# Performance work log

Hardware: AMD Instinct MI355X
Metric: run time of the kernel (lower is better)

Reference implementation:

```python
import jax, jax.numpy as jnp
import numpy as np

N, E, B = 3000, 96000, 64
CIN, MID = 8, 16
G1, G2 = 32, 8
FC1, FC2, OUT = 512, 128, 10
EPS = 1e-5


def setup_inputs() -> dict:
    key = jax.random.key(0)
    ks = jax.random.split(key, 40)
    u = lambda k, shape, s: jax.random.uniform(k, shape, jnp.float32, -s, s)
    inp = {}
    inp['x'] = jax.random.normal(ks[0], (N, B, CIN), jnp.float32)
    inp['edge_index'] = jax.random.randint(ks[1], (2, E), 0, N, jnp.int64)
    # SAGEConv params (uniform(-1/sqrt(in_channels), ...))
    s = 1.0 / np.sqrt(CIN)
    inp['edge_w_raw'] = jnp.ones((E,), jnp.float32) * 0.01
    inp['sage_self_w'] = u(ks[2], (CIN, MID), s)
    inp['sage_w'] = u(ks[3], (CIN, MID), s)
    inp['sage_b'] = u(ks[4], (MID,), s)
    # LayerNorm over (num_nodes, mid_channel)
    inp['ln_g'] = jnp.ones((N, MID), jnp.float32)
    inp['ln_b'] = jnp.zeros((N, MID), jnp.float32)
    # 1x1 Conv2d stacks (stored as [out,in] matrices) + BatchNorm2d (eval stats)
    inp['conv1_w'] = jax.random.normal(ks[5], (G1, MID), jnp.float32) * np.sqrt(2.0 / G1)
    inp['conv1_b'] = u(ks[6], (G1,), 1.0 / np.sqrt(MID))
    inp['bn1_g'] = jax.random.uniform(ks[7], (G1,), jnp.float32, 0.5, 1.5)
    inp['bn1_b'] = jax.random.normal(ks[8], (G1,), jnp.float32) * 0.1
    inp['bn1_m'] = jax.random.normal(ks[9], (G1,), jnp.float32) * 0.1
    inp['bn1_v'] = jax.random.uniform(ks[10], (G1,), jnp.float32, 0.5, 1.5)
    inp['conv2_w'] = jax.random.normal(ks[11], (G2, G1), jnp.float32) * np.sqrt(2.0 / G2)
    inp['conv2_b'] = u(ks[12], (G2,), 1.0 / np.sqrt(G1))
    inp['bn2_g'] = jax.random.uniform(ks[13], (G2,), jnp.float32, 0.5, 1.5)
    inp['bn2_b'] = jax.random.normal(ks[14], (G2,), jnp.float32) * 0.1
    inp['bn2_m'] = jax.random.normal(ks[15], (G2,), jnp.float32) * 0.1
    inp['bn2_v'] = jax.random.uniform(ks[16], (G2,), jnp.float32, 0.5, 1.5)
    # FC stack: Linear(G2*N, FC1) + BN1d, Linear(FC1, FC2) + BN1d, fc1
    d0 = G2 * N
    inp['fc_w1'] = jax.random.normal(ks[17], (FC1, d0), jnp.float32) * np.sqrt(2.0 / (d0 + FC1))
    inp['fc_b1'] = jnp.full((FC1,), 0.01, jnp.float32)
    inp['bnf1_g'] = jax.random.uniform(ks[18], (FC1,), jnp.float32, 0.5, 1.5)
    inp['bnf1_b'] = jax.random.normal(ks[19], (FC1,), jnp.float32) * 0.1
    inp['bnf1_m'] = jax.random.normal(ks[20], (FC1,), jnp.float32) * 0.1
    inp['bnf1_v'] = jax.random.uniform(ks[21], (FC1,), jnp.float32, 0.5, 1.5)
    inp['fc_w2'] = jax.random.normal(ks[22], (FC2, FC1), jnp.float32) * np.sqrt(2.0 / (FC1 + FC2))
    inp['fc_b2'] = jnp.full((FC2,), 0.01, jnp.float32)
    inp['bnf2_g'] = jax.random.uniform(ks[23], (FC2,), jnp.float32, 0.5, 1.5)
    inp['bnf2_b'] = jax.random.normal(ks[24], (FC2,), jnp.float32) * 0.1
    inp['bnf2_m'] = jax.random.normal(ks[25], (FC2,), jnp.float32) * 0.1
    inp['bnf2_v'] = jax.random.uniform(ks[26], (FC2,), jnp.float32, 0.5, 1.5)
    inp['fc1_w'] = jax.random.normal(ks[27], (OUT, FC2), jnp.float32) * np.sqrt(2.0 / (FC2 + OUT))
    inp['fc1_b'] = jnp.full((OUT,), 0.01, jnp.float32)
    return inp


def _bn(y, g, b, m, v):
    # eval-mode BatchNorm; y is [B, C, N] or [B, C]
    if y.ndim == 3:
        return (y - m[:, None]) * (g[:, None] / jnp.sqrt(v[:, None] + EPS)) + b[:, None]
    return (y - m) * (g / jnp.sqrt(v + EPS)) + b


def reference(x, edge_index, edge_w_raw, sage_self_w, sage_w, sage_b, ln_g, ln_b,
              conv1_w, conv1_b, bn1_g, bn1_b, bn1_m, bn1_v,
              conv2_w, conv2_b, bn2_g, bn2_b, bn2_m, bn2_v,
              fc_w1, fc_b1, bnf1_g, bnf1_b, bnf1_m, bnf1_v,
              fc_w2, fc_b2, bnf2_g, bnf2_b, bnf2_m, bnf2_v,
              fc1_w, fc1_b):
    row, col = edge_index[0], edge_index[1]
    ew = jax.nn.sigmoid(edge_w_raw)
    # SAGEConv: gather -> weighted message -> scatter-mean by col -> matmul
    msg = x[row] * ew[:, None, None]                          # [E, B, CIN]
    summed = jax.ops.segment_sum(msg, col, num_segments=N)    # [N, B, CIN]
    cnt = jax.ops.segment_sum(jnp.ones((E,), x.dtype), col, num_segments=N)
    agg = summed / jnp.maximum(cnt, 1.0)[:, None, None]
    neigh = jnp.einsum('nbc,cm->nbm', agg, sage_w) + sage_b   # [N, B, MID]
    self_out = jnp.einsum('nbc,cm->nbm', x, sage_self_w)
    h = 0.0 * self_out + 1.0 * neigh                          # alphas = [0, 1]
    h = jax.nn.relu(h)
    # LayerNorm over (num_nodes, mid) per batch element
    hb = jnp.transpose(h, (1, 0, 2))                          # [B, N, MID]
    mu = hb.mean(axis=(1, 2), keepdims=True)
    var = hb.var(axis=(1, 2), keepdims=True)
    hb = (hb - mu) / jnp.sqrt(var + EPS) * ln_g + ln_b
    y = jnp.transpose(hb, (0, 2, 1))                          # [B, MID, N]
    # 1x1 conv stack (relu then BN, matching source order)
    y = jnp.einsum('om,bmn->bon', conv1_w, y) + conv1_b[:, None]
    y = _bn(jax.nn.relu(y), bn1_g, bn1_b, bn1_m, bn1_v)
    y = jnp.einsum('oc,bcn->bon', conv2_w, y) + conv2_b[:, None]
    y = _bn(jax.nn.relu(y), bn2_g, bn2_b, bn2_m, bn2_v)       # [B, G2, N]
    z = y.reshape(y.shape[0], -1)                             # [B, G2*N]
    z = jax.nn.relu(_bn(z @ fc_w1.T + fc_b1, bnf1_g, bnf1_b, bnf1_m, bnf1_v))
    z = jax.nn.relu(_bn(z @ fc_w2.T + fc_b2, bnf2_g, bnf2_b, bnf2_m, bnf2_v))
    logits = z @ fc1_w.T + fc1_b
    return jax.nn.softmax(logits, axis=-1), logits
```

## Files before the change

kernel.cpp:

```cpp
#include <hip/hip_runtime.h>
#include <hip/hip_bf16.h>
#include <math.h>

#define NN   3000
#define EE   96000
#define BB   64
#define CIN  8
#define MID  16
#define G1   32
#define G2   8
#define FC1N 512
#define FC2N 128
#define OUTN 10
#define EPSV 1e-5f

#define BC   (BB * CIN)
#define HROW (NN * MID)
#define D0   (G2 * NN)

#define P_EWRAW 0
#define P_SW    96000
#define P_SB    96128
#define P_LNG   96144
#define P_LNB   144144
#define P_C1W   192144
#define P_C1B   192656
#define P_BN1G  192688
#define P_BN1B  192720
#define P_BN1M  192752
#define P_BN1V  192784
#define P_C2W   192816
#define P_C2B   193072
#define P_BN2G  193080
#define P_BN2B  193088
#define P_BN2M  193096
#define P_BN2V  193104
#define P_FB1   193112
#define P_BF1G  193624
#define P_BF1B  194136
#define P_BF1M  194648
#define P_BF1V  195160
#define P_FW2   195672
#define P_FB2   261208
#define P_BF2G  261336
#define P_BF2B  261464
#define P_BF2M  261592
#define P_BF2V  261720
#define P_FOW   261848
#define P_FOB   263128
#define P_TOT   263138

#define KCH  320
#define NKC  75

__device__ __forceinline__ float b2f(unsigned short u) {
    union { unsigned int i; float f; } c;
    c.i = ((unsigned int)u) << 16;
    return c.f;
}
__device__ __forceinline__ unsigned short f2b_rne(float x) {
    union { float f; unsigned int u; } c; c.f = x;
    unsigned int r = c.u + 0x7FFFu + ((c.u >> 16) & 1u);
    return (unsigned short)(r >> 16);
}

typedef __attribute__((ext_vector_type(8))) short short8;
typedef __attribute__((ext_vector_type(4))) float f32x4;

struct PTab { const void* p[30]; };
__global__ __launch_bounds__(256)
void k_prep(const void* __restrict__ ei_raw, const unsigned int* __restrict__ ewr,
            PTab tab,
            int* __restrict__ ei32, int* __restrict__ cnt, int* __restrict__ flags,
            float* __restrict__ P) {
    __shared__ int sh_is64, sh_bf;
    if (threadIdx.x == 0) {
        const int* pw = (const int*)ei_raw;
        int any = 0;
        #pragma unroll
        for (int i = 1; i < 32; i += 2) any |= pw[i];
        sh_is64 = (any == 0) ? 1 : 0;
        unsigned int w = ewr[0];
        sh_bf = ((w >> 16) == (w & 0xFFFFu)) ? 1 : 0;
        if (blockIdx.x == 0) flags[0] = sh_bf;
    }
    __syncthreads();
    int bf = sh_bf;
    long long gi = (long long)blockIdx.x * blockDim.x + threadIdx.x;
    if (gi < 2 * EE) {
        int i = (int)gi;
        int v = sh_is64 ? (int)((const long long*)ei_raw)[i]
                        : ((const int*)ei_raw)[i];
        ei32[i] = v;
        if (i >= EE) atomicAdd(&cnt[v], 1);
        return;
    }
    gi -= 2 * EE;
    if (gi >= P_TOT) return;
    int i = (int)gi;
    const int off[31] = {
        P_EWRAW, P_SW, P_SB, P_LNG, P_LNB, P_C1W, P_C1B, P_BN1G, P_BN1B, P_BN1M,
        P_BN1V, P_C2W, P_C2B, P_BN2G, P_BN2B, P_BN2M, P_BN2V, P_FB1, P_BF1G,
        P_BF1B, P_BF1M, P_BF1V, P_FW2, P_FB2, P_BF2G, P_BF2B, P_BF2M, P_BF2V,
        P_FOW, P_FOB, P_TOT };
    int r = 0;
    #pragma unroll
    for (int j = 1; j < 31; ++j) r += (i >= off[j]) ? 1 : 0;
    int e = i - off[r];
    P[i] = bf ? b2f(((const unsigned short*)tab.p[r])[e])
              : ((const float*)tab.p[r])[e];
}

__global__ void k_scan(const int* __restrict__ cnt, int* __restrict__ off,
                       int* __restrict__ cursor) {
    __shared__ int part[1024];
    int t = threadIdx.x;
    int base = t * 3;
    int c0 = 0, c1 = 0, c2 = 0;
    if (base     < NN) c0 = cnt[base];
    if (base + 1 < NN) c1 = cnt[base + 1];
    if (base + 2 < NN) c2 = cnt[base + 2];
    int s = c0 + c1 + c2;
    part[t] = s;
    __syncthreads();
    for (int d = 1; d < 1024; d <<= 1) {
        int v = (t >= d) ? part[t - d] : 0;
        __syncthreads();
        part[t] += v;
        __syncthreads();
    }
    int excl = part[t] - s;
    if (base < NN)     { off[base]     = excl;           cursor[base]     = excl; }
    if (base + 1 < NN) { off[base + 1] = excl + c0;      cursor[base + 1] = excl + c0; }
    if (base + 2 < NN) { off[base + 2] = excl + c0 + c1; cursor[base + 2] = excl + c0 + c1; }
    if (t == 1023) off[NN] = part[1023];
}

__global__ void k_scatter(const int* __restrict__ ei, const float* __restrict__ ew,
                          int* __restrict__ cursor,
                          int* __restrict__ rcsr, float* __restrict__ wcsr) {
    int e = blockIdx.x * blockDim.x + threadIdx.x;
    if (e < EE) {
        int p = atomicAdd(&cursor[ei[EE + e]], 1);
        rcsr[p] = ei[e];
        wcsr[p] = 1.f / (1.f + expf(-ew[e]));
    }
}

__global__ __launch_bounds__(256)
void k_agg_sage(const void* __restrict__ xraw, const int* __restrict__ flags,
                const int* __restrict__ off,
                const int* __restrict__ rcsr, const float* __restrict__ wcsr,
                const float* __restrict__ sw, const float* __restrict__ sb,
                float* __restrict__ hb,
                float* __restrict__ statsS, float* __restrict__ statsQ) {
    __shared__ float aggL[BC];
    __shared__ float swL[CIN * MID];
    __shared__ float sbL[MID];
    __shared__ float lnS[BB], lnQ[BB];
    int t = threadIdx.x;
    if (t < CIN * MID) swL[t] = sw[t];
    if (t < MID)       sbL[t] = sb[t];
    if (t < BB) { lnS[t] = 0.f; lnQ[t] = 0.f; }
    int bf = flags[0];
    float accS[4] = {0.f, 0.f, 0.f, 0.f};
    float accQ[4] = {0.f, 0.f, 0.f, 0.f};
    __syncthreads();
    for (int j = 0; j < 4; ++j) {
        int n = blockIdx.x * 4 + j;
        int k0 = off[n], k1 = off[n + 1];
        float a0 = 0.f, a1 = 0.f, b0 = 0.f, b1 = 0.f;
        int k = k0;
        if (bf) {
            const unsigned int* xu = (const unsigned int*)xraw;
            for (; k + 3 < k1; k += 4) {
                int   r0 = rcsr[k],     r1 = rcsr[k + 1];
                int   r2 = rcsr[k + 2], r3 = rcsr[k + 3];
                float w0 = wcsr[k],     w1 = wcsr[k + 1];
                float w2 = wcsr[k + 2], w3 = wcsr[k + 3];
                unsigned int u0 = xu[(size_t)r0 * 256 + t];
                unsigned int u1 = xu[(size_t)r1 * 256 + t];
                unsigned int u2 = xu[(size_t)r2 * 256 + t];
                unsigned int u3 = xu[(size_t)r3 * 256 + t];
                a0 += b2f((unsigned short)(u0 & 0xFFFFu)) * w0;
                a1 += b2f((unsigned short)(u0 >> 16))     * w0;
                b0 += b2f((unsigned short)(u1 & 0xFFFFu)) * w1;
                b1 += b2f((unsigned short)(u1 >> 16))     * w1;
                a0 += b2f((unsigned short)(u2 & 0xFFFFu)) * w2;
                a1 += b2f((unsigned short)(u2 >> 16))     * w2;
                b0 += b2f((unsigned short)(u3 & 0xFFFFu)) * w3;
                b1 += b2f((unsigned short)(u3 >> 16))     * w3;
            }
            for (; k < k1; ++k) {
                int r0 = rcsr[k];
                float w0 = wcsr[k];
                unsigned int u0 = xu[(size_t)r0 * 256 + t];
                a0 += b2f((unsigned short)(u0 & 0xFFFFu)) * w0;
                a1 += b2f((unsigned short)(u0 >> 16))     * w0;
            }
        } else {
            const float* x = (const float*)xraw;
            for (; k + 3 < k1; k += 4) {
                int   r0 = rcsr[k],     r1 = rcsr[k + 1];
                int   r2 = rcsr[k + 2], r3 = rcsr[k + 3];
                float w0 = wcsr[k],     w1 = wcsr[k + 1];
                float w2 = wcsr[k + 2], w3 = wcsr[k + 3];
                const float* xp0 = x + (size_t)r0 * BC;
                const float* xp1 = x + (size_t)r1 * BC;
                const float* xp2 = x + (size_t)r2 * BC;
                const float* xp3 = x + (size_t)r3 * BC;
                a0 += xp0[t] * w0;  a1 += xp0[t + 256] * w0;
                b0 += xp1[t] * w1;  b1 += xp1[t + 256] * w1;
                a0 += xp2[t] * w2;  a1 += xp2[t + 256] * w2;
                b0 += xp3[t] * w3;  b1 += xp3[t + 256] * w3;
            }
            for (; k < k1; ++k) {
                int r0 = rcsr[k];
                float w0 = wcsr[k];
                const float* xp0 = x + (size_t)r0 * BC;
                a0 += xp0[t] * w0;
                a1 += xp0[t + 256] * w0;
            }
        }
        float inv = 1.f / fmaxf((float)(k1 - k0), 1.f);
        __syncthreads();
        if (bf) {
            aggL[2 * t]     = (a0 + b0) * inv;
            aggL[2 * t + 1] = (a1 + b1) * inv;
        } else {
            aggL[t]       = (a0 + b0) * inv;
            aggL[t + 256] = (a1 + b1) * inv;
        }
        __syncthreads();
        #pragma unroll
        for (int r4 = 0; r4 < 4; ++r4) {
            int q = t + r4 * 256;
            int b = q >> 4, m = q & 15;
            float v = sbL[m];
            const float* ag = &aggL[b * CIN];
            #pragma unroll
            for (int c = 0; c < CIN; ++c) v += ag[c] * swL[c * MID + m];
            v = fmaxf(v, 0.f);
            hb[(size_t)b * HROW + n * MID + m] = v;
            accS[r4] += v;
            accQ[r4] += v * v;
        }
    }
    __syncthreads();
    #pragma unroll
    for (int r4 = 0; r4 < 4; ++r4) {
        int b = (t + r4 * 256) >> 4;
        atomicAdd(&lnS[b], accS[r4]);
        atomicAdd(&lnQ[b], accQ[r4]);
    }
    __syncthreads();
    if (t < BB) {
        atomicAdd(&statsS[t], lnS[t]);
        atomicAdd(&statsQ[t], lnQ[t]);
    }
}

__global__ __launch_bounds__(256)
void k_conv_stack(const float* __restrict__ hb,
                  const float* __restrict__ statsS, const float* __restrict__ statsQ,
                  const float* __restrict__ P, unsigned short* __restrict__ zT) {
    __shared__ float hbt[64 * 65];
    __shared__ float w1s[G1 * MID], w2s[G2 * G1];
    __shared__ float c1s[G1], s1[G1], t1[G1];
    __shared__ float c2s[G2], s2[G2], t2[G2];
    int t = threadIdx.x;
    int n0 = blockIdx.x * 4;
    for (int j = t; j < G1 * MID; j += 256) w1s[j] = P[P_C1W + j];
    if (t < G2 * G1)  w2s[t] = P[P_C2W + t];
    if (t < G1) {
        float s = P[P_BN1G + t] / sqrtf(P[P_BN1V + t] + EPSV);
        c1s[t] = P[P_C1B + t]; s1[t] = s; t1[t] = P[P_BN1B + t] - P[P_BN1M + t] * s;
    }
    if (t < G2) {
        float s = P[P_BN2G + t] / sqrtf(P[P_BN2V + t] + EPSV);
        c2s[t] = P[P_C2B + t]; s2[t] = s; t2[t] = P[P_BN2B + t] - P[P_BN2M + t] * s;
    }
    #pragma unroll
    for (int r = 0; r < 4; ++r) {
        int i = r * 256 + t;
        int b = i >> 4, q = i & 15;
        float4 v = *(const float4*)(hb + (size_t)b * HROW + n0 * MID + q * 4);
        int ld = b * 65 + q * 4;
        hbt[ld] = v.x; hbt[ld + 1] = v.y; hbt[ld + 2] = v.z; hbt[ld + 3] = v.w;
    }
    __syncthreads();
    int nl = t >> 6, b = t & 63;
    int n = n0 + nl;
    float mu = statsS[b] / (float)HROW;
    float var = statsQ[b] / (float)HROW - mu * mu;
    float rs = 1.f / sqrtf(var + EPSV);
    float tv[MID];
    #pragma unroll
    for (int m = 0; m < MID; ++m) {
        float g = P[P_LNG + n * MID + m], lb = P[P_LNB + n * MID + m];
        tv[m] = (hbt[b * 65 + nl * MID + m] - mu) * rs * g + lb;
    }
    float v1[G1];
    #pragma unroll
    for (int o = 0; o < G1; ++o) {
        float d = c1s[o];
        #pragma unroll
        for (int m = 0; m < MID; ++m) d += w1s[o * MID + m] * tv[m];
        d = fmaxf(d, 0.f);
        v1[o] = d * s1[o] + t1[o];
    }
    #pragma unroll
    for (int o2 = 0; o2 < G2; ++o2) {
        float d = c2s[o2];
        #pragma unroll
        for (int c = 0; c < G1; ++c) d += w2s[o2 * G1 + c] * v1[c];
        d = fmaxf(d, 0.f);
        zT[((size_t)(o2 * NN + n)) * BB + b] = f2b_rne(d * s2[o2] + t2[o2]);
    }
}

__global__ __launch_bounds__(256)
void k_fc1(const unsigned short* __restrict__ zT, const void* __restrict__ w1raw,
           const int* __restrict__ flags, float* __restrict__ out1p) {
    __shared__ unsigned int zs[64 * 20];
    int kc = blockIdx.y;
    int t = threadIdx.x;
    int lane = t & 63;
    int wv = t >> 6;
    int n = lane & 15;
    int q = lane >> 4;
    int fbase = blockIdx.x * 64 + wv * 16;
    int bf = flags[0];
    const size_t kcb = (size_t)kc * KCH;
    const float*          w1f = (const float*)w1raw;
    const unsigned short* w1b = (const unsigned short*)w1raw;

    f32x4 acc0 = {0.f, 0.f, 0.f, 0.f};
    f32x4 acc1 = {0.f, 0.f, 0.f, 0.f};
    f32x4 acc2 = {0.f, 0.f, 0.f, 0.f};
    f32x4 acc3 = {0.f, 0.f, 0.f, 0.f};

    int zb = t & 63;
    int kg = t >> 6;

    for (int ks = 0; ks < KCH / 32; ++ks) {
        size_t k0 = kcb + (size_t)ks * 32;
        const unsigned short* zsrc = zT + (k0 + kg * 8) * BB + zb;
        unsigned short zv[8];
        #pragma unroll
        for (int j = 0; j < 8; ++j) zv[j] = zsrc[j * BB];
        unsigned int pk0 = (unsigned int)zv[0] | ((unsigned int)zv[1] << 16);
        unsigned int pk1 = (unsigned int)zv[2] | ((unsigned int)zv[3] << 16);
        unsigned int pk2 = (unsigned int)zv[4] | ((unsigned int)zv[5] << 16);
        unsigned int pk3 = (unsigned int)zv[6] | ((unsigned int)zv[7] << 16);
        __syncthreads();
        *(uint4*)&zs[zb * 20 + kg * 4] = make_uint4(pk0, pk1, pk2, pk3);
        short8 av;
        if (bf) {
            av = *(const short8*)(w1b + (size_t)(fbase + n) * D0 + k0 + q * 8);
        } else {
            const float* wr = w1f + (size_t)(fbase + n) * D0 + k0 + q * 8;
            float4 wa = *(const float4*)wr;
            float4 wb = *(const float4*)(wr + 4);
            av[0] = (short)f2b_rne(wa.x); av[1] = (short)f2b_rne(wa.y);
            av[2] = (short)f2b_rne(wa.z); av[3] = (short)f2b_rne(wa.w);
            av[4] = (short)f2b_rne(wb.x); av[5] = (short)f2b_rne(wb.y);
            av[6] = (short)f2b_rne(wb.z); av[7] = (short)f2b_rne(wb.w);
        }
        __syncthreads();
        const char* zbase = (const char*)zs + q * 16;
        short8 bv0 = *(const short8*)(zbase + (0  + n) * 80);
        short8 bv1 = *(const short8*)(zbase + (16 + n) * 80);
        short8 bv2 = *(const short8*)(zbase + (32 + n) * 80);
        short8 bv3 = *(const short8*)(zbase + (48 + n) * 80);
        acc0 = __builtin_amdgcn_mfma_f32_16x16x32_bf16(av, bv0, acc0, 0, 0, 0);
        acc1 = __builtin_amdgcn_mfma_f32_16x16x32_bf16(av, bv1, acc1, 0, 0, 0);
        acc2 = __builtin_amdgcn_mfma_f32_16x16x32_bf16(av, bv2, acc2, 0, 0, 0);
        acc3 = __builtin_amdgcn_mfma_f32_16x16x32_bf16(av, bv3, acc3, 0, 0, 0);
    }
    float* op = out1p + ((size_t)kc * FC1N + fbase + q * 4) * BB + n;
    #pragma unroll
    for (int r = 0; r < 4; ++r) {
        op[r * BB +  0] = acc0[r];
        op[r * BB + 16] = acc1[r];
        op[r * BB + 32] = acc2[r];
        op[r * BB + 48] = acc3[r];
    }
}

__global__ void k_fc1_fin(const float* __restrict__ out1p, const float* __restrict__ P,
                          float* __restrict__ z1) {
    int i = blockIdx.x * blockDim.x + threadIdx.x;
    if (i < BB * FC1N) {
        int f = i >> 6, b = i & 63;
        float acc = 0.f;
        for (int kc = 0; kc < NKC; ++kc)
            acc += out1p[((size_t)kc * FC1N + f) * BB + b];
        acc += P[P_FB1 + f];
        float s = P[P_BF1G + f] / sqrtf(P[P_BF1V + f] + EPSV);
        acc = (acc - P[P_BF1M + f]) * s + P[P_BF1B + f];
        z1[b * FC1N + f] = fmaxf(acc, 0.f);
    }
}

__global__ __launch_bounds__(128)
void k_fc2head(const float* __restrict__ z1, const float* __restrict__ P,
               const int* __restrict__ flags, void* __restrict__ outv) {
    __shared__ float zsrc[FC1N];
    __shared__ float z2s[FC2N];
    __shared__ float lg[OUTN];
    __shared__ float red[2];
    int b = blockIdx.x, t = threadIdx.x;
    #pragma unroll
    for (int r = 0; r < 4; ++r) zsrc[t + r * 128] = z1[b * FC1N + t + r * 128];
    __syncthreads();
    {
        int f = t;
        const float4* wr = (const float4*)(P + P_FW2 + (size_t)f * FC1N);
        const float4* zr = (const float4*)zsrc;
        float acc = P[P_FB2 + f];
        for (int k = 0; k < FC1N / 4; ++k) {
            float4 wv = wr[k];
            float4 zv = zr[k];
            acc += wv.x * zv.x + wv.y * zv.y + wv.z * zv.z + wv.w * zv.w;
        }
        float s = P[P_BF2G + f] / sqrtf(P[P_BF2V + f] + EPSV);
        acc = (acc - P[P_BF2M + f]) * s + P[P_BF2B + f];
        z2s[f] = fmaxf(acc, 0.f);
    }
    __syncthreads();
    if (t < OUTN) {
        float acc = P[P_FOB + t];
        const float* wr = P + P_FOW + t * FC2N;
        for (int k = 0; k < FC2N; ++k) acc += wr[k] * z2s[k];
        lg[t] = acc;
    }
    __syncthreads();
    if (t == 0) {
        float mx = lg[0];
        for (int o = 1; o < OUTN; ++o) mx = fmaxf(mx, lg[o]);
        float s = 0.f;
        for (int o = 0; o < OUTN; ++o) s += expf(lg[o] - mx);
        red[0] = mx; red[1] = s;
    }
    __syncthreads();
    if (t < OUTN) {
        float p = expf(lg[t] - red[0]) / red[1];
        if (flags[0]) {
            __hip_bfloat16* o = (__hip_bfloat16*)outv;
            o[b * OUTN + t] = __float2bfloat16(p);
            o[BB * OUTN + b * OUTN + t] = __float2bfloat16(lg[t]);
        } else {
            float* o = (float*)outv;
            o[b * OUTN + t] = p;
            o[BB * OUTN + b * OUTN + t] = lg[t];
        }
    }
}

extern "C" void kernel_launch(void* const* d_in, const int* in_sizes, int n_in,
                              void* d_out, int out_size, void* d_ws, size_t ws_size,
                              hipStream_t stream) {
    char* ws = (char*)d_ws;
    size_t o = 0;
    auto carve = [&](size_t bytes) { void* p = ws + o; o += (bytes + 255) & ~(size_t)255; return p; };
    int*   flags  = (int*)  carve(16);
    int*   ei32   = (int*)  carve((size_t)2 * EE * sizeof(int));
    int*   cnt    = (int*)  carve(NN * sizeof(int));
    float* statsS = (float*)carve(BB * sizeof(float));
    float* statsQ = (float*)carve(BB * sizeof(float));
    int*   off    = (int*)  carve((NN + 1) * sizeof(int));
    int*   cursor = (int*)  carve(NN * sizeof(int));
    int*   rcsr   = (int*)  carve(EE * sizeof(int));
    float* wcsr   = (float*)carve(EE * sizeof(float));
    float* P      = (float*)carve((size_t)P_TOT * sizeof(float));
    float* hb     = (float*)carve((size_t)BB * HROW * sizeof(float));
    unsigned short* zT = (unsigned short*)carve((size_t)D0 * BB * sizeof(unsigned short));
    float* out1p  = (float*)carve((size_t)NKC * FC1N * BB * sizeof(float));
    float* z1     = (float*)carve(BB * FC1N * sizeof(float));

    size_t zero_bytes = ((NN * sizeof(int) + 255) & ~(size_t)255)
                      + 2 * ((BB * sizeof(float) + 255) & ~(size_t)255);
    hipMemsetAsync(cnt, 0, zero_bytes, stream);

    PTab tab;
    tab.p[0]  = d_in[2];   tab.p[1]  = d_in[4];   tab.p[2]  = d_in[5];
    tab.p[3]  = d_in[6];   tab.p[4]  = d_in[7];   tab.p[5]  = d_in[8];
    tab.p[6]  = d_in[9];   tab.p[7]  = d_in[10];  tab.p[8]  = d_in[11];
    tab.p[9]  = d_in[12];  tab.p[10] = d_in[13];  tab.p[11] = d_in[14];
    tab.p[12] = d_in[15];  tab.p[13] = d_in[16];  tab.p[14] = d_in[17];
    tab.p[15] = d_in[18];  tab.p[16] = d_in[19];  tab.p[17] = d_in[21];
    tab.p[18] = d_in[22];  tab.p[19] = d_in[23];  tab.p[20] = d_in[24];
    tab.p[21] = d_in[25];  tab.p[22] = d_in[26];  tab.p[23] = d_in[27];
    tab.p[24] = d_in[28];  tab.p[25] = d_in[29];  tab.p[26] = d_in[30];
    tab.p[27] = d_in[31];  tab.p[28] = d_in[32];  tab.p[29] = d_in[33];

    long long prep_tot = 2LL * EE + P_TOT;
    k_prep<<<(int)((prep_tot + 255) / 256), 256, 0, stream>>>(
        d_in[1], (const unsigned int*)d_in[2], tab, ei32, cnt, flags, P);

    k_scan   <<<1, 1024, 0, stream>>>(cnt, off, cursor);
    k_scatter<<<(EE + 255) / 256, 256, 0, stream>>>(ei32, P + P_EWRAW, cursor, rcsr, wcsr);
    k_agg_sage<<<NN / 4, 256, 0, stream>>>(d_in[0], flags, off, rcsr, wcsr,
                                           P + P_SW, P + P_SB, hb, statsS, statsQ);
    k_conv_stack<<<NN / 4, 256, 0, stream>>>(hb, statsS, statsQ, P, zT);
    dim3 g7(FC1N / 64, NKC);
    k_fc1    <<<g7, 256, 0, stream>>>(zT, d_in[20], flags, out1p);
    k_fc1_fin<<<(BB * FC1N + 255) / 256, 256, 0, stream>>>(out1p, P, z1);
    k_fc2head<<<BB, 128, 0, stream>>>(z1, P, flags, (void*)d_out);
}
```

Before: 268.7 us.

## Map one wavefront per node in SAGE aggregation with vector loads and node-major layout

The aggregation kernel now assigns each wavefront one destination node, and each lane owns one batch element's 8 channels. Neighbor rows are read with 16-byte vector loads, and the SAGE linear, ReLU and LayerNorm statistics are computed in registers, which removes the shared-memory staging and per-node block barriers. The intermediate h buffer moves from batch-major to node-major layout [N][B][MID] so stores are contiguous float4 writes, and the conv stack's loads are rewritten to match. Per-thread register use grows, and per-lane LDS atomics on the statistics replace the earlier grouped atomics.

```diff
diff --git a/kernel.cpp b/kernel.cpp
--- a/kernel.cpp
+++ b/kernel.cpp
@@ -63,6 +63,16 @@
     unsigned int r = c.u + 0x7FFFu + ((c.u >> 16) & 1u);
     return (unsigned short)(r >> 16);
 }
+__device__ __forceinline__ void acc_bf16x8(float* a, uint4 u, float w) {
+    a[0] += b2f((unsigned short)(u.x & 0xFFFFu)) * w;
+    a[1] += b2f((unsigned short)(u.x >> 16))     * w;
+    a[2] += b2f((unsigned short)(u.y & 0xFFFFu)) * w;
+    a[3] += b2f((unsigned short)(u.y >> 16))     * w;
+    a[4] += b2f((unsigned short)(u.z & 0xFFFFu)) * w;
+    a[5] += b2f((unsigned short)(u.z >> 16))     * w;
+    a[6] += b2f((unsigned short)(u.w & 0xFFFFu)) * w;
+    a[7] += b2f((unsigned short)(u.w >> 16))     * w;
+}
 
 typedef __attribute__((ext_vector_type(8))) short short8;
 typedef __attribute__((ext_vector_type(4))) float f32x4;
@@ -152,9 +162,8 @@
                 const int* __restrict__ off,
                 const int* __restrict__ rcsr, const float* __restrict__ wcsr,
                 const float* __restrict__ sw, const float* __restrict__ sb,
-                float* __restrict__ hb,
+                float* __restrict__ hb2,
                 float* __restrict__ statsS, float* __restrict__ statsQ) {
-    __shared__ float aggL[BC];
     __shared__ float swL[CIN * MID];
     __shared__ float sbL[MID];
     __shared__ float lnS[BB], lnQ[BB];
@@ -162,97 +171,79 @@
     if (t < CIN * MID) swL[t] = sw[t];
     if (t < MID)       sbL[t] = sb[t];
     if (t < BB) { lnS[t] = 0.f; lnQ[t] = 0.f; }
-    int bf = flags[0];
-    float accS[4] = {0.f, 0.f, 0.f, 0.f};
-    float accQ[4] = {0.f, 0.f, 0.f, 0.f};
-    __syncthreads();
-    for (int j = 0; j < 4; ++j) {
-        int n = blockIdx.x * 4 + j;
-        int k0 = off[n], k1 = off[n + 1];
-        float a0 = 0.f, a1 = 0.f, b0 = 0.f, b1 = 0.f;
-        int k = k0;
-        if (bf) {
-            const unsigned int* xu = (const unsigned int*)xraw;
-            for (; k + 3 < k1; k += 4) {
-                int   r0 = rcsr[k],     r1 = rcsr[k + 1];
-                int   r2 = rcsr[k + 2], r3 = rcsr[k + 3];
-                float w0 = wcsr[k],     w1 = wcsr[k + 1];
-                float w2 = wcsr[k + 2], w3 = wcsr[k + 3];
-                unsigned int u0 = xu[(size_t)r0 * 256 + t];
-                unsigned int u1 = xu[(size_t)r1 * 256 + t];
-                unsigned int u2 = xu[(size_t)r2 * 256 + t];
-                unsigned int u3 = xu[(size_t)r3 * 256 + t];
-                a0 += b2f((unsigned short)(u0 & 0xFFFFu)) * w0;
-                a1 += b2f((unsigned short)(u0 >> 16))     * w0;
-                b0 += b2f((unsigned short)(u1 & 0xFFFFu)) * w1;
-                b1 += b2f((unsigned short)(u1 >> 16))     * w1;
-                a0 += b2f((unsigned short)(u2 & 0xFFFFu)) * w2;
-                a1 += b2f((unsigned short)(u2 >> 16))     * w2;
-                b0 += b2f((unsigned short)(u3 & 0xFFFFu)) * w3;
-                b1 += b2f((unsigned short)(u3 >> 16))     * w3;
-            }
-            for (; k < k1; ++k) {
-                int r0 = rcsr[k];
-                float w0 = wcsr[k];
-                unsigned int u0 = xu[(size_t)r0 * 256 + t];
-                a0 += b2f((unsigned short)(u0 & 0xFFFFu)) * w0;
-                a1 += b2f((unsigned short)(u0 >> 16))     * w0;
-            }
-        } else {
-            const float* x = (const float*)xraw;
-            for (; k + 3 < k1; k += 4) {
-                int   r0 = rcsr[k],     r1 = rcsr[k + 1];
-                int   r2 = rcsr[k + 2], r3 = rcsr[k + 3];
-                float w0 = wcsr[k],     w1 = wcsr[k + 1];
-                float w2 = wcsr[k + 2], w3 = wcsr[k + 3];
-                const float* xp0 = x + (size_t)r0 * BC;
-                const float* xp1 = x + (size_t)r1 * BC;
-                const float* xp2 = x + (size_t)r2 * BC;
-                const float* xp3 = x + (size_t)r3 * BC;
-                a0 += xp0[t] * w0;  a1 += xp0[t + 256] * w0;
-                b0 += xp1[t] * w1;  b1 += xp1[t + 256] * w1;
-                a0 += xp2[t] * w2;  a1 += xp2[t + 256] * w2;
-                b0 += xp3[t] * w3;  b1 += xp3[t + 256] * w3;
-            }
-            for (; k < k1; ++k) {
-                int r0 = rcsr[k];
-                float w0 = wcsr[k];
-                const float* xp0 = x + (size_t)r0 * BC;
-                a0 += xp0[t] * w0;
-                a1 += xp0[t + 256] * w0;
-            }
-        }
-        float inv = 1.f / fmaxf((float)(k1 - k0), 1.f);
-        __syncthreads();
-        if (bf) {
-            aggL[2 * t]     = (a0 + b0) * inv;
-            aggL[2 * t + 1] = (a1 + b1) * inv;
-        } else {
-            aggL[t]       = (a0 + b0) * inv;
-            aggL[t + 256] = (a1 + b1) * inv;
-        }
-        __syncthreads();
+    __syncthreads();
+    int wv = t >> 6, lane = t & 63;
+    int n = blockIdx.x * 4 + wv;
+    int k0 = off[n], k1 = off[n + 1];
+    float a[8];
+    #pragma unroll
+    for (int c = 0; c < 8; ++c) a[c] = 0.f;
+    int k = k0;
+    if (flags[0]) {
+        const uint4* xu = (const uint4*)xraw;
+        for (; k + 3 < k1; k += 4) {
+            int   r0 = rcsr[k],     r1 = rcsr[k + 1];
+            int   r2 = rcsr[k + 2], r3 = rcsr[k + 3];
+            float w0 = wcsr[k],     w1 = wcsr[k + 1];
+            float w2 = wcsr[k + 2], w3 = wcsr[k + 3];
+            uint4 u0 = xu[(size_t)r0 * 64 + lane];
+            uint4 u1 = xu[(size_t)r1 * 64 + lane];
+            uint4 u2 = xu[(size_t)r2 * 64 + lane];
+            uint4 u3 = xu[(size_t)r3 * 64 + lane];
+            acc_bf16x8(a, u0, w0);
+            acc_bf16x8(a, u1, w1);
+            acc_bf16x8(a, u2, w2);
+            acc_bf16x8(a, u3, w3);
+        }
+        for (; k < k1; ++k) {
+            uint4 u0 = xu[(size_t)rcsr[k] * 64 + lane];
+            acc_bf16x8(a, u0, wcsr[k]);
+        }
+    } else {
+        const float4* xf = (const float4*)xraw;
+        for (; k + 1 < k1; k += 2) {
+            int   r0 = rcsr[k],   r1 = rcsr[k + 1];
+            float w0 = wcsr[k],   w1 = wcsr[k + 1];
+            float4 f0 = xf[(size_t)r0 * 128 + lane * 2];
+            float4 f1 = xf[(size_t)r0 * 128 + lane * 2 + 1];
+            float4 g0 = xf[(size_t)r1 * 128 + lane * 2];
+            float4 g1 = xf[(size_t)r1 * 128 + lane * 2 + 1];
+            a[0] += f0.x * w0 + g0.x * w1;  a[1] += f0.y * w0 + g0.y * w1;
+            a[2] += f0.z * w0 + g0.z * w1;  a[3] += f0.w * w0 + g0.w * w1;
+            a[4] += f1.x * w0 + g1.x * w1;  a[5] += f1.y * w0 + g1.y * w1;
+            a[6] += f1.z * w0 + g1.z * w1;  a[7] += f1.w * w0 + g1.w * w1;
+        }
+        if (k < k1) {
+            float w0 = wcsr[k];
+            float4 f0 = xf[(size_t)rcsr[k] * 128 + lane * 2];
+            float4 f1 = xf[(size_t)rcsr[k] * 128 + lane * 2 + 1];
+            a[0] += f0.x * w0;  a[1] += f0.y * w0;
+            a[2] += f0.z * w0;  a[3] += f0.w * w0;
+            a[4] += f1.x * w0;  a[5] += f1.y * w0;
+            a[6] += f1.z * w0;  a[7] += f1.w * w0;
+        }
+    }
+    float inv = 1.f / fmaxf((float)(k1 - k0), 1.f);
+    #pragma unroll
+    for (int c = 0; c < 8; ++c) a[c] *= inv;
+    float accS = 0.f, accQ = 0.f;
+    float ov[MID];
+    #pragma unroll
+    for (int m = 0; m < MID; ++m) {
+        float v = sbL[m];
         #pragma unroll
-        for (int r4 = 0; r4 < 4; ++r4) {
-            int q = t + r4 * 256;
-            int b = q >> 4, m = q & 15;
-            float v = sbL[m];
-            const float* ag = &aggL[b * CIN];
-            #pragma unroll
-            for (int c = 0; c < CIN; ++c) v += ag[c] * swL[c * MID + m];
-            v = fmaxf(v, 0.f);
-            hb[(size_t)b * HROW + n * MID + m] = v;
-            accS[r4] += v;
-            accQ[r4] += v * v;
-        }
-    }
-    __syncthreads();
-    #pragma unroll
-    for (int r4 = 0; r4 < 4; ++r4) {
-        int b = (t + r4 * 256) >> 4;
-        atomicAdd(&lnS[b], accS[r4]);
-        atomicAdd(&lnQ[b], accQ[r4]);
-    }
+        for (int c = 0; c < CIN; ++c) v += a[c] * swL[c * MID + m];
+        v = fmaxf(v, 0.f);
+        ov[m] = v;
+        accS += v;
+        accQ += v * v;
+    }
+    float* hp = hb2 + (size_t)n * 1024 + lane * 16;
+    #pragma unroll
+    for (int m4 = 0; m4 < 4; ++m4)
+        *(float4*)(hp + m4 * 4) = make_float4(ov[m4*4], ov[m4*4+1], ov[m4*4+2], ov[m4*4+3]);
+    atomicAdd(&lnS[lane], accS);
+    atomicAdd(&lnQ[lane], accQ);
     __syncthreads();
     if (t < BB) {
         atomicAdd(&statsS[t], lnS[t]);
@@ -261,7 +252,7 @@
 }
 
 __global__ __launch_bounds__(256)
-void k_conv_stack(const float* __restrict__ hb,
+void k_conv_stack(const float* __restrict__ hb2,
                   const float* __restrict__ statsS, const float* __restrict__ statsQ,
                   const float* __restrict__ P, unsigned short* __restrict__ zT) {
     __shared__ float hbt[64 * 65];
@@ -282,10 +273,10 @@
     }
     #pragma unroll
     for (int r = 0; r < 4; ++r) {
-        int i = r * 256 + t;
-        int b = i >> 4, q = i & 15;
-        float4 v = *(const float4*)(hb + (size_t)b * HROW + n0 * MID + q * 4);
-        int ld = b * 65 + q * 4;
+        int j = t;
+        float4 v = *(const float4*)(hb2 + (size_t)(n0 + r) * 1024 + j * 4);
+        int b = j >> 2, m4 = j & 3;
+        int ld = b * 65 + r * 16 + m4 * 4;
         hbt[ld] = v.x; hbt[ld + 1] = v.y; hbt[ld + 2] = v.z; hbt[ld + 3] = v.w;
     }
     __syncthreads();
@@ -298,7 +289,7 @@
     #pragma unroll
     for (int m = 0; m < MID; ++m) {
         float g = P[P_LNG + n * MID + m], lb = P[P_LNB + n * MID + m];
-        tv[m] = (hbt[b * 65 + nl * MID + m] - mu) * rs * g + lb;
+        tv[m] = (hbt[b * 65 + nl * 16 + m] - mu) * rs * g + lb;
     }
     float v1[G1];
     #pragma unroll
@@ -474,7 +465,7 @@
     int*   rcsr   = (int*)  carve(EE * sizeof(int));
     float* wcsr   = (float*)carve(EE * sizeof(float));
     float* P      = (float*)carve((size_t)P_TOT * sizeof(float));
-    float* hb     = (float*)carve((size_t)BB * HROW * sizeof(float));
+    float* hb2    = (float*)carve((size_t)NN * 1024 * sizeof(float));
     unsigned short* zT = (unsigned short*)carve((size_t)D0 * BB * sizeof(unsigned short));
     float* out1p  = (float*)carve((size_t)NKC * FC1N * BB * sizeof(float));
     float* z1     = (float*)carve(BB * FC1N * sizeof(float));
@@ -502,8 +493,8 @@
     k_scan   <<<1, 1024, 0, stream>>>(cnt, off, cursor);
     k_scatter<<<(EE + 255) / 256, 256, 0, stream>>>(ei32, P + P_EWRAW, cursor, rcsr, wcsr);
     k_agg_sage<<<NN / 4, 256, 0, stream>>>(d_in[0], flags, off, rcsr, wcsr,
-                                           P + P_SW, P + P_SB, hb, statsS, statsQ);
-    k_conv_stack<<<NN / 4, 256, 0, stream>>>(hb, statsS, statsQ, P, zT);
+                                           P + P_SW, P + P_SB, hb2, statsS, statsQ);
+    k_conv_stack<<<NN / 4, 256, 0, stream>>>(hb2, statsS, statsQ, P, zT);
     dim3 g7(FC1N / 64, NKC);
     k_fc1    <<<g7, 256, 0, stream>>>(zT, d_in[20], flags, out1p);
     k_fc1_fin<<<(BB * FC1N + 255) / 256, 256, 0, stream>>>(out1p, P, z1);
```

New measurement: 260.4 us. -3.1%, faster.
